# Kernel optimization log

Hardware: AMD Instinct MI355X
Metric: run time of the kernel (lower is better)

The kernel has to match this reference:

```python
import jax, jax.numpy as jnp
import numpy as np

MOMENTUM_DECAY = 0.9
AMP_THRESHOLD = 0.1
CORR_THRESHOLD = 0.3
MAX_STEERING = 0.5
EPS = 1e-12  # torch F.normalize eps


def _normalize(x):
    return x / jnp.maximum(jnp.linalg.norm(x), EPS)


def setup_inputs() -> dict:
    key = jax.random.key(0)
    k1, k2, k3 = jax.random.split(key, 3)
    B, S, D = 1, 8192, 4096
    return {
        "hidden_states": jax.random.normal(k1, (B, S, D), dtype=jnp.float32),
        "correct_direction": jax.random.normal(k2, (D,), dtype=jnp.float32),
        "incorrect_direction": jax.random.normal(k3, (D,), dtype=jnp.float32),
        "steering_scale": jnp.ones((1,), dtype=jnp.float32),
    }


def reference(hidden_states, correct_direction, incorrect_direction, steering_scale):
    B, S, D = hidden_states.shape
    # reasoning quality: cosine sims of pooled state against reference directions
    current = hidden_states.mean(axis=1)[0]              # [D] (batch assumed 1)
    current_norm = _normalize(current)
    csim = jnp.where(jnp.linalg.norm(correct_direction) > 0,
                     jnp.dot(current_norm, correct_direction), 0.0)
    isim = jnp.where(jnp.linalg.norm(incorrect_direction) > 0,
                     jnp.dot(current_norm, incorrect_direction), 0.0)
    quality = csim - isim
    steering_dir = _normalize(correct_direction - incorrect_direction)
    # fresh state: momentum_vector is None -> momentum = steering_dir
    momentum = steering_dir
    # adaptive alpha (piecewise in quality)
    amp_alpha = MAX_STEERING * (AMP_THRESHOLD - quality) / (AMP_THRESHOLD + CORR_THRESHOLD)
    alpha = jnp.where(quality < -CORR_THRESHOLD, MAX_STEERING,
                      jnp.where(quality < AMP_THRESHOLD, amp_alpha, 0.05))
    # vectorized per-position steering (replaces the Python for-loop)
    rel_pos = jnp.arange(S, dtype=hidden_states.dtype) / S     # [S]
    pos_weight = 0.5 + 0.5 * rel_pos                           # [S]
    eff_alpha = alpha * pos_weight * steering_scale[0]         # [S]
    delta = eff_alpha[:, None] * momentum[None, :]             # [S, D]
    dnorm = jnp.linalg.norm(delta, axis=-1, keepdims=True)     # [S, 1]
    delta = jnp.where(dnorm > MAX_STEERING, delta * (MAX_STEERING / dnorm), delta)
    return hidden_states + delta[None, :, :]
```

## Files before the change

kernel.cpp:

```cpp
#include <hip/hip_runtime.h>
#include <math.h>

#define EPSV 1e-12f

__global__ void ara_colsum(const float* __restrict__ hid, float* __restrict__ sums,
                           int D4, int rows_per_chunk) {
    int d4 = blockIdx.x * blockDim.x + threadIdx.x;
    if (d4 >= D4) return;
    long row0 = (long)blockIdx.y * rows_per_chunk;
    const float4* h4 = reinterpret_cast<const float4*>(hid);
    float4 acc = make_float4(0.f, 0.f, 0.f, 0.f);
    for (int r = 0; r < rows_per_chunk; ++r) {
        float4 v = h4[(row0 + r) * D4 + d4];
        acc.x += v.x; acc.y += v.y; acc.z += v.z; acc.w += v.w;
    }
    atomicAdd(&sums[4 * d4 + 0], acc.x);
    atomicAdd(&sums[4 * d4 + 1], acc.y);
    atomicAdd(&sums[4 * d4 + 2], acc.z);
    atomicAdd(&sums[4 * d4 + 3], acc.w);
}

__global__ void ara_scalars(const float* __restrict__ sums, const float* __restrict__ cdir,
                            const float* __restrict__ idir, const float* __restrict__ sscale,
                            float* __restrict__ scal, int D, int S) {
    float sc2 = 0.f, si2 = 0.f, scd = 0.f, sid = 0.f, scur2 = 0.f, sd2 = 0.f;
    for (int d = threadIdx.x; d < D; d += blockDim.x) {
        float c = cdir[d], ii = idir[d], sm = sums[d];
        sc2 += c * c; si2 += ii * ii;
        scd += sm * c; sid += sm * ii;
        scur2 += sm * sm;
        float df = c - ii; sd2 += df * df;
    }
    float vals[6] = {sc2, si2, scd, sid, scur2, sd2};
    __shared__ float red[6][4];
    int lane = threadIdx.x & 63;
    int wid = threadIdx.x >> 6;
#pragma unroll
    for (int k = 0; k < 6; ++k) {
        float v = vals[k];
#pragma unroll
        for (int o = 32; o > 0; o >>= 1) v += __shfl_down(v, o, 64);
        if (lane == 0) red[k][wid] = v;
    }
    __syncthreads();
    if (threadIdx.x == 0) {
        float t[6];
#pragma unroll
        for (int k = 0; k < 6; ++k) t[k] = red[k][0] + red[k][1] + red[k][2] + red[k][3];
        float invS = 1.0f / (float)S;
        float cn = sqrtf(t[4]) * invS;
        float inv_cn = 1.0f / fmaxf(cn, EPSV);
        float csim = (sqrtf(t[0]) > 0.f) ? (t[2] * invS * inv_cn) : 0.f;
        float isim = (sqrtf(t[1]) > 0.f) ? (t[3] * invS * inv_cn) : 0.f;
        float quality = csim - isim;
        float amp = 0.5f * (0.1f - quality) / (0.1f + 0.3f);
        float alpha = (quality < -0.3f) ? 0.5f : ((quality < 0.1f) ? amp : 0.05f);
        float ndiff = sqrtf(t[5]);
        float inv_nd = 1.0f / fmaxf(ndiff, EPSV);
        scal[0] = alpha * sscale[0];
        scal[1] = inv_nd;
        scal[2] = ndiff * inv_nd;
    }
}

__global__ void ara_apply(const float* __restrict__ hid, const float* __restrict__ cdir,
                          const float* __restrict__ idir, const float* __restrict__ scal,
                          float* __restrict__ out, int D4, int S, long total4) {
    float a_s = scal[0], inv_nd = scal[1], mnorm = scal[2];
    float invS = 1.0f / (float)S;
    const float4* h4 = reinterpret_cast<const float4*>(hid);
    const float4* c4 = reinterpret_cast<const float4*>(cdir);
    const float4* i4 = reinterpret_cast<const float4*>(idir);
    float4* o4 = reinterpret_cast<float4*>(out);
    long stride = (long)gridDim.x * blockDim.x;
    for (long idx = (long)blockIdx.x * blockDim.x + threadIdx.x; idx < total4; idx += stride) {
        long s = idx / D4;
        int d4 = (int)(idx - s * D4);
        float eff = a_s * (0.5f + 0.5f * ((float)s * invS));
        float dn = fabsf(eff) * mnorm;
        float coef = (dn > 0.5f) ? (eff * (0.5f / dn)) : eff;
        coef *= inv_nd;
        float4 h = h4[idx], c = c4[d4], i = i4[d4];
        float4 r;
        r.x = h.x + coef * (c.x - i.x);
        r.y = h.y + coef * (c.y - i.y);
        r.z = h.z + coef * (c.z - i.z);
        r.w = h.w + coef * (c.w - i.w);
        o4[idx] = r;
    }
}

extern "C" void kernel_launch(void* const* d_in, const int* in_sizes, int n_in,
                              void* d_out, int out_size, void* d_ws, size_t ws_size,
                              hipStream_t stream) {
    const float* hid    = (const float*)d_in[0];
    const float* cdir   = (const float*)d_in[1];
    const float* idir   = (const float*)d_in[2];
    const float* sscale = (const float*)d_in[3];
    float* out = (float*)d_out;

    int D = in_sizes[1];
    long total = (long)in_sizes[0];
    int S = (int)(total / D);
    int D4 = D / 4;

    float* sums = (float*)d_ws;
    float* scal = sums + D;

    hipMemsetAsync(d_ws, 0, (size_t)D * sizeof(float), stream);

    int rows_per_chunk = 64;
    dim3 g1((D4 + 255) / 256, (S + rows_per_chunk - 1) / rows_per_chunk);
    ara_colsum<<<g1, 256, 0, stream>>>(hid, sums, D4, rows_per_chunk);

    ara_scalars<<<1, 256, 0, stream>>>(sums, cdir, idir, sscale, scal, D, S);

    long total4 = total / 4;
    ara_apply<<<4096, 256, 0, stream>>>(hid, cdir, idir, scal, out, D4, S, total4);
}
```

Baseline: 93.04 us.

## Fuse colsum, scalar reduction and apply into one cooperative kernel with grid syncs

Replaces the memset plus three kernel launches with a single cooperative kernel of 1024 blocks. It zeroes sums, accumulates column sums, then has every block redundantly compute the scalar coefficients before applying steering, with grid syncs between phases. The apply phase caches the normalized momentum vector in registers and processes contiguous row ranges per block. This removes launch overhead and the serial single-block scalar kernel, but adds grid-sync cost and redundant per-block reductions. The register cache only covers D4 up to 1024, because mv[j&3] wraps for larger D4.

```diff
diff --git a/kernel.cpp b/kernel.cpp
--- a/kernel.cpp
+++ b/kernel.cpp
@@ -1,92 +1,133 @@
 #include <hip/hip_runtime.h>
+#include <hip/hip_cooperative_groups.h>
 #include <math.h>
+
+namespace cg = cooperative_groups;
 
 #define EPSV 1e-12f
 
-__global__ void ara_colsum(const float* __restrict__ hid, float* __restrict__ sums,
-                           int D4, int rows_per_chunk) {
-    int d4 = blockIdx.x * blockDim.x + threadIdx.x;
-    if (d4 >= D4) return;
-    long row0 = (long)blockIdx.y * rows_per_chunk;
+__global__ __launch_bounds__(256, 4)
+void ara_fused(const float* __restrict__ hid, const float* __restrict__ cdir,
+               const float* __restrict__ idir, const float* __restrict__ sscale,
+               float* __restrict__ out, float* __restrict__ sums,
+               int S, int D4) {
+    cg::grid_group grid = cg::this_grid();
     const float4* h4 = reinterpret_cast<const float4*>(hid);
-    float4 acc = make_float4(0.f, 0.f, 0.f, 0.f);
-    for (int r = 0; r < rows_per_chunk; ++r) {
-        float4 v = h4[(row0 + r) * D4 + d4];
-        acc.x += v.x; acc.y += v.y; acc.z += v.z; acc.w += v.w;
+    const float4* c4p = reinterpret_cast<const float4*>(cdir);
+    const float4* i4p = reinterpret_cast<const float4*>(idir);
+    const float4* s4p = reinterpret_cast<const float4*>(sums);
+    float4* o4 = reinterpret_cast<float4*>(out);
+
+    const int tid = threadIdx.x;
+    const int bid = blockIdx.x;
+    const int nthreads = gridDim.x * blockDim.x;
+    const int gt = bid * blockDim.x + tid;
+    const int D = D4 * 4;
+
+    for (int i = gt; i < D; i += nthreads) sums[i] = 0.f;
+    grid.sync();
+
+    {
+        int nchunk = nthreads / D4;
+        int rows_per_chunk = (S + nchunk - 1) / nchunk;
+        int c4 = gt % D4;
+        int chunk = gt / D4;
+        long row0 = (long)chunk * rows_per_chunk;
+        float4 acc = make_float4(0.f, 0.f, 0.f, 0.f);
+        for (int r = 0; r < rows_per_chunk; ++r) {
+            long row = row0 + r;
+            if (row < S) {
+                float4 v = h4[row * (long)D4 + c4];
+                acc.x += v.x; acc.y += v.y; acc.z += v.z; acc.w += v.w;
+            }
+        }
+        atomicAdd(&sums[4 * c4 + 0], acc.x);
+        atomicAdd(&sums[4 * c4 + 1], acc.y);
+        atomicAdd(&sums[4 * c4 + 2], acc.z);
+        atomicAdd(&sums[4 * c4 + 3], acc.w);
     }
-    atomicAdd(&sums[4 * d4 + 0], acc.x);
-    atomicAdd(&sums[4 * d4 + 1], acc.y);
-    atomicAdd(&sums[4 * d4 + 2], acc.z);
-    atomicAdd(&sums[4 * d4 + 3], acc.w);
-}
+    grid.sync();
 
-__global__ void ara_scalars(const float* __restrict__ sums, const float* __restrict__ cdir,
-                            const float* __restrict__ idir, const float* __restrict__ sscale,
-                            float* __restrict__ scal, int D, int S) {
-    float sc2 = 0.f, si2 = 0.f, scd = 0.f, sid = 0.f, scur2 = 0.f, sd2 = 0.f;
-    for (int d = threadIdx.x; d < D; d += blockDim.x) {
-        float c = cdir[d], ii = idir[d], sm = sums[d];
-        sc2 += c * c; si2 += ii * ii;
-        scd += sm * c; sid += sm * ii;
-        scur2 += sm * sm;
-        float df = c - ii; sd2 += df * df;
+    __shared__ float red[6][4];
+    __shared__ float bcast[3];
+    {
+        float sc2 = 0.f, si2 = 0.f, scd = 0.f, sid = 0.f, scur2 = 0.f, sd2 = 0.f;
+        for (int d4 = tid; d4 < D4; d4 += blockDim.x) {
+            float4 c = c4p[d4], iv = i4p[d4], sm = s4p[d4];
+            sc2 += c.x * c.x + c.y * c.y + c.z * c.z + c.w * c.w;
+            si2 += iv.x * iv.x + iv.y * iv.y + iv.z * iv.z + iv.w * iv.w;
+            scd += sm.x * c.x + sm.y * c.y + sm.z * c.z + sm.w * c.w;
+            sid += sm.x * iv.x + sm.y * iv.y + sm.z * iv.z + sm.w * iv.w;
+            scur2 += sm.x * sm.x + sm.y * sm.y + sm.z * sm.z + sm.w * sm.w;
+            float dx = c.x - iv.x, dy = c.y - iv.y, dz = c.z - iv.z, dw = c.w - iv.w;
+            sd2 += dx * dx + dy * dy + dz * dz + dw * dw;
+        }
+        float vals[6] = {sc2, si2, scd, sid, scur2, sd2};
+        int lane = tid & 63;
+        int wid = tid >> 6;
+#pragma unroll
+        for (int k = 0; k < 6; ++k) {
+            float v = vals[k];
+#pragma unroll
+            for (int o = 32; o > 0; o >>= 1) v += __shfl_down(v, o, 64);
+            if (lane == 0) red[k][wid] = v;
+        }
+        __syncthreads();
+        if (tid == 0) {
+            float t[6];
+#pragma unroll
+            for (int k = 0; k < 6; ++k)
+                t[k] = red[k][0] + red[k][1] + red[k][2] + red[k][3];
+            float invS = 1.0f / (float)S;
+            float cn = sqrtf(t[4]) * invS;
+            float inv_cn = 1.0f / fmaxf(cn, EPSV);
+            float csim = (sqrtf(t[0]) > 0.f) ? (t[2] * invS * inv_cn) : 0.f;
+            float isim = (sqrtf(t[1]) > 0.f) ? (t[3] * invS * inv_cn) : 0.f;
+            float quality = csim - isim;
+            float amp = 0.5f * (0.1f - quality) / (0.1f + 0.3f);
+            float alpha = (quality < -0.3f) ? 0.5f : ((quality < 0.1f) ? amp : 0.05f);
+            float ndiff = sqrtf(t[5]);
+            float inv_nd = 1.0f / fmaxf(ndiff, EPSV);
+            bcast[0] = alpha * sscale[0];
+            bcast[1] = inv_nd;
+            bcast[2] = ndiff * inv_nd;
+        }
+        __syncthreads();
     }
-    float vals[6] = {sc2, si2, scd, sid, scur2, sd2};
-    __shared__ float red[6][4];
-    int lane = threadIdx.x & 63;
-    int wid = threadIdx.x >> 6;
-#pragma unroll
-    for (int k = 0; k < 6; ++k) {
-        float v = vals[k];
-#pragma unroll
-        for (int o = 32; o > 0; o >>= 1) v += __shfl_down(v, o, 64);
-        if (lane == 0) red[k][wid] = v;
-    }
-    __syncthreads();
-    if (threadIdx.x == 0) {
-        float t[6];
-#pragma unroll
-        for (int k = 0; k < 6; ++k) t[k] = red[k][0] + red[k][1] + red[k][2] + red[k][3];
-        float invS = 1.0f / (float)S;
-        float cn = sqrtf(t[4]) * invS;
-        float inv_cn = 1.0f / fmaxf(cn, EPSV);
-        float csim = (sqrtf(t[0]) > 0.f) ? (t[2] * invS * inv_cn) : 0.f;
-        float isim = (sqrtf(t[1]) > 0.f) ? (t[3] * invS * inv_cn) : 0.f;
-        float quality = csim - isim;
-        float amp = 0.5f * (0.1f - quality) / (0.1f + 0.3f);
-        float alpha = (quality < -0.3f) ? 0.5f : ((quality < 0.1f) ? amp : 0.05f);
-        float ndiff = sqrtf(t[5]);
-        float inv_nd = 1.0f / fmaxf(ndiff, EPSV);
-        scal[0] = alpha * sscale[0];
-        scal[1] = inv_nd;
-        scal[2] = ndiff * inv_nd;
-    }
-}
+    const float a_s = bcast[0], inv_nd = bcast[1], mnorm = bcast[2];
+    const float invS = 1.0f / (float)S;
 
-__global__ void ara_apply(const float* __restrict__ hid, const float* __restrict__ cdir,
-                          const float* __restrict__ idir, const float* __restrict__ scal,
-                          float* __restrict__ out, int D4, int S, long total4) {
-    float a_s = scal[0], inv_nd = scal[1], mnorm = scal[2];
-    float invS = 1.0f / (float)S;
-    const float4* h4 = reinterpret_cast<const float4*>(hid);
-    const float4* c4 = reinterpret_cast<const float4*>(cdir);
-    const float4* i4 = reinterpret_cast<const float4*>(idir);
-    float4* o4 = reinterpret_cast<float4*>(out);
-    long stride = (long)gridDim.x * blockDim.x;
-    for (long idx = (long)blockIdx.x * blockDim.x + threadIdx.x; idx < total4; idx += stride) {
-        long s = idx / D4;
-        int d4 = (int)(idx - s * D4);
-        float eff = a_s * (0.5f + 0.5f * ((float)s * invS));
-        float dn = fabsf(eff) * mnorm;
-        float coef = (dn > 0.5f) ? (eff * (0.5f / dn)) : eff;
-        coef *= inv_nd;
-        float4 h = h4[idx], c = c4[d4], i = i4[d4];
-        float4 r;
-        r.x = h.x + coef * (c.x - i.x);
-        r.y = h.y + coef * (c.y - i.y);
-        r.z = h.z + coef * (c.z - i.z);
-        r.w = h.w + coef * (c.w - i.w);
-        o4[idx] = r;
+    {
+        int rows_per_block = (S + gridDim.x - 1) / gridDim.x;
+        long row0 = (long)bid * rows_per_block;
+        int jcols = D4 >> 8;
+        float4 mv[4];
+        for (int j = 0; j < jcols && j < 4; ++j) {
+            int d4 = (j << 8) + tid;
+            float4 c = c4p[d4], iv = i4p[d4];
+            mv[j].x = (c.x - iv.x) * inv_nd;
+            mv[j].y = (c.y - iv.y) * inv_nd;
+            mv[j].z = (c.z - iv.z) * inv_nd;
+            mv[j].w = (c.w - iv.w) * inv_nd;
+        }
+        for (int r = 0; r < rows_per_block; ++r) {
+            long s = row0 + r;
+            if (s >= S) break;
+            float eff = a_s * (0.5f + 0.5f * ((float)s * invS));
+            float dn = fabsf(eff) * mnorm;
+            float coef = (dn > 0.5f) ? (eff * (0.5f / dn)) : eff;
+            for (int j = 0; j < jcols; ++j) {
+                long idx = s * (long)D4 + (j << 8) + tid;
+                float4 h = h4[idx];
+                float4 m = mv[j & 3];
+                float4 rr;
+                rr.x = h.x + coef * m.x;
+                rr.y = h.y + coef * m.y;
+                rr.z = h.z + coef * m.z;
+                rr.w = h.w + coef * m.w;
+                o4[idx] = rr;
+            }
+        }
     }
 }
 
@@ -105,16 +146,9 @@
     int D4 = D / 4;
 
     float* sums = (float*)d_ws;
-    float* scal = sums + D;
 
-    hipMemsetAsync(d_ws, 0, (size_t)D * sizeof(float), stream);
-
-    int rows_per_chunk = 64;
-    dim3 g1((D4 + 255) / 256, (S + rows_per_chunk - 1) / rows_per_chunk);
-    ara_colsum<<<g1, 256, 0, stream>>>(hid, sums, D4, rows_per_chunk);
-
-    ara_scalars<<<1, 256, 0, stream>>>(sums, cdir, idir, sscale, scal, D, S);
-
-    long total4 = total / 4;
-    ara_apply<<<4096, 256, 0, stream>>>(hid, cdir, idir, scal, out, D4, S, total4);
+    dim3 grid(1024), block(256);
+    void* args[] = { (void*)&hid, (void*)&cdir, (void*)&idir, (void*)&sscale,
+                     (void*)&out, (void*)&sums, (void*)&S, (void*)&D4 };
+    hipLaunchCooperativeKernel((void*)ara_fused, grid, block, args, 0, stream);
 }
```

Result: slower. 258.9 us (+178.3%).
